# Kernel optimization log

Measured on AMD Instinct MI355X. Metric: run time of the kernel, lower is better.

Reference implementation:

```python
import jax, jax.numpy as jnp
import numpy as np

MARGIN = 0.5
EPS = 1e-12  # matches torch F.normalize eps


def setup_inputs() -> dict:
    key = jax.random.key(0)
    embeddings = jax.random.normal(key, (8192, 256), dtype=jnp.float32)
    return {"embeddings": embeddings}


def reference(embeddings):
    n = embeddings.shape[0]
    # L2-normalize rows (torch F.normalize: x / max(||x||, eps))
    norm = jnp.linalg.norm(embeddings, axis=1, keepdims=True)
    e = embeddings / jnp.maximum(norm, EPS)
    sim = e @ e.T  # [n, n]
    # strict upper triangle mask (i < j)
    iu = jnp.triu(jnp.ones((n, n), dtype=bool), k=1)
    loss_sum = jnp.sum(jnp.where(iu, jax.nn.relu(sim - MARGIN), 0.0))
    count = n * (n - 1) // 2
    return loss_sum / count
```

## Files before the change

### kernel.cpp

```cpp
#include <hip/hip_runtime.h>
#include <hip/hip_fp16.h>

typedef __attribute__((ext_vector_type(4))) float f32x4;
typedef __attribute__((ext_vector_type(8))) int i32x8;

#define NROWS 8192
#define DCOLS 256
#define MARGIN 0.5f
#define NBAND 128
#define NCT 64
#define NBLOCKS 1088

__global__ __launch_bounds__(256) void norm_kernel(const float* __restrict__ x,
                                                   unsigned char* __restrict__ e) {
    const int t = threadIdx.x;
    const int l = t & 63;
    const int c = l & 31;
    const int row = blockIdx.x * 8 + (t >> 6) * 2 + (l >> 5);

    const float4 v0 = *reinterpret_cast<const float4*>(&x[row * DCOLS + c * 8]);
    const float4 v1 = *reinterpret_cast<const float4*>(&x[row * DCOLS + c * 8 + 4]);
    float ss = v0.x * v0.x + v0.y * v0.y + v0.z * v0.z + v0.w * v0.w
             + v1.x * v1.x + v1.y * v1.y + v1.z * v1.z + v1.w * v1.w;
#pragma unroll
    for (int off = 16; off >= 1; off >>= 1) ss += __shfl_xor(ss, off, 32);
    const float inv = 1.0f / fmaxf(sqrtf(ss), 1e-12f);

    const float f[8] = {v0.x, v0.y, v0.z, v0.w, v1.x, v1.y, v1.z, v1.w};
    unsigned int lo = 0, hi = 0;
#pragma unroll
    for (int i = 0; i < 4; ++i) {
        const unsigned short hb = __half_as_ushort(__float2half(f[i] * inv));
        lo |= (unsigned int)(hb >> 8) << (8 * i);
    }
#pragma unroll
    for (int i = 0; i < 4; ++i) {
        const unsigned short hb = __half_as_ushort(__float2half(f[4 + i] * inv));
        hi |= (unsigned int)(hb >> 8) << (8 * i);
    }
    uint2 o; o.x = lo; o.y = hi;
    *reinterpret_cast<uint2*>(e + (size_t)row * DCOLS + c * 8) = o;
}

__global__ __launch_bounds__(256, 4) void tile_kernel(const unsigned char* __restrict__ e,
                                                      float* __restrict__ part) {
    const int orig = blockIdx.x;
    int bb = (orig & 7) * 136 + (orig >> 3);
    int bi = 0, r;
    while (bb >= (r = ((NCT - (bi >> 1)) + 3) >> 2)) { bb -= r; ++bi; }
    const int j0 = (bi >> 1) + bb * 4;
    const int nj = min(4, NCT - j0);
    const int NS = nj * 2;

    __shared__ char lds[40960];
    char* As = lds;
    char* Bw = lds + 8192;

    const int t = threadIdx.x;
    const int l = t & 63;
    const int w = t >> 6;
    const int wn = w;
    const int lr = l & 15;
    const int hk = l >> 4;
    const unsigned char* eA = e + (size_t)bi * 64 * DCOLS;
    char* myB = Bw + w * 8192;

    auto stageB = [&](int s, int slot) {
        const int jt = j0 + (s >> 1);
        const int kb = s & 1;
        const unsigned char* src = e + (size_t)(jt * 128 + wn * 32) * DCOLS + kb * 128;
#pragma unroll
        for (int i = 0; i < 4; ++i) {
            const int u = i * 64 + l;
            const int hk2 = u >> 6, brow = (u >> 1) & 31, half = u & 1;
            __builtin_amdgcn_global_load_lds(
                (const __attribute__((address_space(1))) void*)(src + brow * DCOLS + hk2 * 32 + half * 16),
                (__attribute__((address_space(3))) void*)(myB + slot * 4096 + u * 16), 16, 0, 0);
        }
    };
    auto stageA = [&](int kb) {
#pragma unroll
        for (int i = 0; i < 2; ++i) {
            const int u = i * 256 + t;
            const int hk2 = u >> 7, arow = (u >> 1) & 63, half = u & 1;
            __builtin_amdgcn_global_load_lds(
                (const __attribute__((address_space(1))) void*)(eA + arow * DCOLS + kb * 128 + hk2 * 32 + half * 16),
                (__attribute__((address_space(3))) void*)(As + u * 16), 16, 0, 0);
        }
    };

    stageA(0);
    stageB(0, 0);
    stageB(1, 1);
    asm volatile("s_waitcnt vmcnt(8)" ::: "memory");
    __builtin_amdgcn_s_barrier();
    __builtin_amdgcn_sched_barrier(0);

    i32x8 af[2][4];
#pragma unroll
    for (int m = 0; m < 4; ++m)
        af[0][m] = *reinterpret_cast<const i32x8*>(As + hk * 2048 + (m * 16 + lr) * 32);
    __builtin_amdgcn_s_barrier();
    __builtin_amdgcn_sched_barrier(0);
    stageA(1);
    asm volatile("s_waitcnt vmcnt(0)" ::: "memory");
    __builtin_amdgcn_s_barrier();
    __builtin_amdgcn_sched_barrier(0);
#pragma unroll
    for (int m = 0; m < 4; ++m)
        af[1][m] = *reinterpret_cast<const i32x8*>(As + hk * 2048 + (m * 16 + lr) * 32);

    f32x4 acc[4][2];
#pragma unroll
    for (int m = 0; m < 4; ++m)
#pragma unroll
        for (int n = 0; n < 2; ++n)
            acc[m][n] = (f32x4){0.f, 0.f, 0.f, 0.f};

    float local = 0.0f;
    for (int jx = 0; jx < nj; ++jx) {
        const int jt = j0 + jx;
#pragma unroll
        for (int kb = 0; kb < 2; ++kb) {
            const int s = jx * 2 + kb;
            asm volatile("s_waitcnt vmcnt(4)" ::: "memory");
            i32x8 bf[2];
#pragma unroll
            for (int n = 0; n < 2; ++n)
                bf[n] = *reinterpret_cast<const i32x8*>(
                    myB + (s & 1) * 4096 + hk * 1024 + (n * 16 + lr) * 32);
            asm volatile("s_waitcnt lgkmcnt(0)" ::: "memory");
            __builtin_amdgcn_sched_barrier(0);
            if (s + 2 < NS) stageB(s + 2, s & 1);
            __builtin_amdgcn_s_setprio(1);
#pragma unroll
            for (int m = 0; m < 4; ++m)
#pragma unroll
                for (int n = 0; n < 2; ++n)
                    acc[m][n] = __builtin_amdgcn_mfma_scale_f32_16x16x128_f8f6f4(
                        af[kb][m], bf[n], acc[m][n],
                        1, 1,
                        0, 0x7F7F7F7F,
                        0, 0x7F7F7F7F);
            __builtin_amdgcn_s_setprio(0);
        }
        const int gi0 = bi * 64;
        const int gj0 = jt * 128 + wn * 32;
        if (jt == (bi >> 1)) {
#pragma unroll
            for (int m = 0; m < 4; ++m)
#pragma unroll
                for (int n = 0; n < 2; ++n) {
#pragma unroll
                    for (int r2 = 0; r2 < 4; ++r2) {
                        const int gi = gi0 + m * 16 + hk * 4 + r2;
                        const int gj = gj0 + n * 16 + lr;
                        local += (gi < gj) ? fmaxf(acc[m][n][r2] - MARGIN, 0.0f) : 0.0f;
                    }
                    acc[m][n] = (f32x4){0.f, 0.f, 0.f, 0.f};
                }
        } else {
#pragma unroll
            for (int m = 0; m < 4; ++m)
#pragma unroll
                for (int n = 0; n < 2; ++n) {
#pragma unroll
                    for (int r2 = 0; r2 < 4; ++r2)
                        local += fmaxf(acc[m][n][r2] - MARGIN, 0.0f);
                    acc[m][n] = (f32x4){0.f, 0.f, 0.f, 0.f};
                }
        }
    }

#pragma unroll
    for (int off = 32; off >= 1; off >>= 1) local += __shfl_down(local, off);
    __syncthreads();
    float* red = (float*)lds;
    if (l == 0) red[w] = local;
    __syncthreads();
    if (t == 0) part[orig] = red[0] + red[1] + red[2] + red[3];
}

__global__ __launch_bounds__(256) void fin_kernel(const float* __restrict__ part,
                                                  float* __restrict__ out) {
    __shared__ float red[4];
    const int t = threadIdx.x;
    float v = part[t] + part[t + 256] + part[t + 512] + part[t + 768]
            + (t < NBLOCKS - 1024 ? part[t + 1024] : 0.0f);
#pragma unroll
    for (int off = 32; off >= 1; off >>= 1) v += __shfl_down(v, off);
    if ((t & 63) == 0) red[t >> 6] = v;
    __syncthreads();
    if (t == 0) out[0] = (red[0] + red[1] + red[2] + red[3]) / 33550336.0f;
}

extern "C" void kernel_launch(void* const* d_in, const int* in_sizes, int n_in,
                              void* d_out, int out_size, void* d_ws, size_t ws_size,
                              hipStream_t stream) {
    const float* x = (const float*)d_in[0];
    float* out = (float*)d_out;
    unsigned char* e = (unsigned char*)d_ws;
    float* part = (float*)((char*)d_ws + (size_t)NROWS * DCOLS);

    norm_kernel<<<NROWS / 8, 256, 0, stream>>>(x, e);
    tile_kernel<<<NBLOCKS, 256, 0, stream>>>(e, part);
    fin_kernel<<<1, 256, 0, stream>>>(part, out);
}
```

Baseline: 33.00 us.

## Use 8-wave blocks with shared B tiles and triple-buffered LDS staging

The tile kernel moves from 4 waves that each staged a private 32-row B slice to 8 waves arranged 2x4 that share a common 128-row B tile. The B tile is triple-buffered with barrier-synchronised prefetch, and the whole A tile is loaded once up front. Each wave now holds a 2x2 accumulator block instead of 4x2, which lowers register pressure and raises wave count per block. In exchange it adds a block-wide barrier every k-step, and LDS use grows to about 64KB per block, which may limit how many blocks fit on a CU.

```diff
diff --git a/kernel.cpp b/kernel.cpp
--- a/kernel.cpp
+++ b/kernel.cpp
@@ -2,12 +2,12 @@
 #include <hip/hip_fp16.h>
 
 typedef __attribute__((ext_vector_type(4))) float f32x4;
+typedef __attribute__((ext_vector_type(4))) int i32x4;
 typedef __attribute__((ext_vector_type(8))) int i32x8;
 
 #define NROWS 8192
 #define DCOLS 256
 #define MARGIN 0.5f
-#define NBAND 128
 #define NCT 64
 #define NBLOCKS 1088
 
@@ -42,7 +42,7 @@
     *reinterpret_cast<uint2*>(e + (size_t)row * DCOLS + c * 8) = o;
 }
 
-__global__ __launch_bounds__(256, 4) void tile_kernel(const unsigned char* __restrict__ e,
+__global__ __launch_bounds__(512, 4) void tile_kernel(const unsigned char* __restrict__ e,
                                                       float* __restrict__ part) {
     const int orig = blockIdx.x;
     int bb = (orig & 7) * 136 + (orig >> 3);
@@ -52,103 +52,98 @@
     const int nj = min(4, NCT - j0);
     const int NS = nj * 2;
 
-    __shared__ char lds[40960];
-    char* As = lds;
-    char* Bw = lds + 8192;
+    __shared__ char As[16384];
+    __shared__ char Bs[3][16384];
+    __shared__ float red[8];
 
     const int t = threadIdx.x;
     const int l = t & 63;
     const int w = t >> 6;
-    const int wn = w;
+    const int wm = w >> 2;
+    const int wn = w & 3;
     const int lr = l & 15;
     const int hk = l >> 4;
+
     const unsigned char* eA = e + (size_t)bi * 64 * DCOLS;
-    char* myB = Bw + w * 8192;
 
     auto stageB = [&](int s, int slot) {
-        const int jt = j0 + (s >> 1);
-        const int kb = s & 1;
-        const unsigned char* src = e + (size_t)(jt * 128 + wn * 32) * DCOLS + kb * 128;
-#pragma unroll
-        for (int i = 0; i < 4; ++i) {
-            const int u = i * 64 + l;
-            const int hk2 = u >> 6, brow = (u >> 1) & 31, half = u & 1;
+        const int jt = j0 + (s >> 1), kb = s & 1;
+#pragma unroll
+        for (int i = 0; i < 2; ++i) {
+            const int u = i * 512 + t;
+            const int half = u >> 9, shk = (u >> 7) & 3, brow = u & 127;
             __builtin_amdgcn_global_load_lds(
-                (const __attribute__((address_space(1))) void*)(src + brow * DCOLS + hk2 * 32 + half * 16),
-                (__attribute__((address_space(3))) void*)(myB + slot * 4096 + u * 16), 16, 0, 0);
+                (const __attribute__((address_space(1))) void*)(e
+                    + (size_t)(jt * 128 + brow) * DCOLS + kb * 128 + shk * 32 + half * 16),
+                (__attribute__((address_space(3))) void*)(Bs[slot] + u * 16), 16, 0, 0);
         }
     };
-    auto stageA = [&](int kb) {
-#pragma unroll
-        for (int i = 0; i < 2; ++i) {
-            const int u = i * 256 + t;
-            const int hk2 = u >> 7, arow = (u >> 1) & 63, half = u & 1;
-            __builtin_amdgcn_global_load_lds(
-                (const __attribute__((address_space(1))) void*)(eA + arow * DCOLS + kb * 128 + hk2 * 32 + half * 16),
-                (__attribute__((address_space(3))) void*)(As + u * 16), 16, 0, 0);
-        }
-    };
-
-    stageA(0);
+
+#pragma unroll
+    for (int i = 0; i < 2; ++i) {
+        const int u = i * 512 + t;
+        const int kb = u >> 9, half = (u >> 8) & 1, shk = (u >> 6) & 3, arow = u & 63;
+        __builtin_amdgcn_global_load_lds(
+            (const __attribute__((address_space(1))) void*)(eA + arow * DCOLS + kb * 128 + shk * 32 + half * 16),
+            (__attribute__((address_space(3))) void*)(As + u * 16), 16, 0, 0);
+    }
     stageB(0, 0);
     stageB(1, 1);
-    asm volatile("s_waitcnt vmcnt(8)" ::: "memory");
-    __builtin_amdgcn_s_barrier();
-    __builtin_amdgcn_sched_barrier(0);
-
-    i32x8 af[2][4];
-#pragma unroll
-    for (int m = 0; m < 4; ++m)
-        af[0][m] = *reinterpret_cast<const i32x8*>(As + hk * 2048 + (m * 16 + lr) * 32);
-    __builtin_amdgcn_s_barrier();
-    __builtin_amdgcn_sched_barrier(0);
-    stageA(1);
-    asm volatile("s_waitcnt vmcnt(0)" ::: "memory");
-    __builtin_amdgcn_s_barrier();
-    __builtin_amdgcn_sched_barrier(0);
-#pragma unroll
-    for (int m = 0; m < 4; ++m)
-        af[1][m] = *reinterpret_cast<const i32x8*>(As + hk * 2048 + (m * 16 + lr) * 32);
-
-    f32x4 acc[4][2];
-#pragma unroll
-    for (int m = 0; m < 4; ++m)
+
+    f32x4 acc[2][2];
+#pragma unroll
+    for (int m = 0; m < 2; ++m)
 #pragma unroll
         for (int n = 0; n < 2; ++n)
             acc[m][n] = (f32x4){0.f, 0.f, 0.f, 0.f};
 
+    const int abase = hk * 1024 + (wm * 32 + lr) * 16;
+    const int bbase = hk * 2048 + (wn * 32 + lr) * 16;
+
     float local = 0.0f;
+    int sl = 0;
     for (int jx = 0; jx < nj; ++jx) {
         const int jt = j0 + jx;
 #pragma unroll
         for (int kb = 0; kb < 2; ++kb) {
             const int s = jx * 2 + kb;
-            asm volatile("s_waitcnt vmcnt(4)" ::: "memory");
-            i32x8 bf[2];
-#pragma unroll
-            for (int n = 0; n < 2; ++n)
-                bf[n] = *reinterpret_cast<const i32x8*>(
-                    myB + (s & 1) * 4096 + hk * 1024 + (n * 16 + lr) * 32);
-            asm volatile("s_waitcnt lgkmcnt(0)" ::: "memory");
-            __builtin_amdgcn_sched_barrier(0);
-            if (s + 2 < NS) stageB(s + 2, s & 1);
+            asm volatile("s_waitcnt vmcnt(2)" ::: "memory");
+            __builtin_amdgcn_s_barrier();
+            if (s + 2 < NS) {
+                int sl2 = sl + 2; if (sl2 >= 3) sl2 -= 3;
+                stageB(s + 2, sl2);
+            }
+            i32x8 af[2], bf[2];
+#pragma unroll
+            for (int m = 0; m < 2; ++m) {
+                i32x4 lo = *reinterpret_cast<const i32x4*>(As + kb * 8192 + m * 256 + abase);
+                i32x4 hi = *reinterpret_cast<const i32x4*>(As + kb * 8192 + 4096 + m * 256 + abase);
+                af[m] = (i32x8){lo[0], lo[1], lo[2], lo[3], hi[0], hi[1], hi[2], hi[3]};
+            }
+#pragma unroll
+            for (int n = 0; n < 2; ++n) {
+                i32x4 lo = *reinterpret_cast<const i32x4*>(Bs[sl] + n * 256 + bbase);
+                i32x4 hi = *reinterpret_cast<const i32x4*>(Bs[sl] + 8192 + n * 256 + bbase);
+                bf[n] = (i32x8){lo[0], lo[1], lo[2], lo[3], hi[0], hi[1], hi[2], hi[3]};
+            }
             __builtin_amdgcn_s_setprio(1);
 #pragma unroll
-            for (int m = 0; m < 4; ++m)
+            for (int m = 0; m < 2; ++m)
 #pragma unroll
                 for (int n = 0; n < 2; ++n)
                     acc[m][n] = __builtin_amdgcn_mfma_scale_f32_16x16x128_f8f6f4(
-                        af[kb][m], bf[n], acc[m][n],
+                        af[m], bf[n], acc[m][n],
                         1, 1,
                         0, 0x7F7F7F7F,
                         0, 0x7F7F7F7F);
             __builtin_amdgcn_s_setprio(0);
+            ++sl; if (sl >= 3) sl -= 3;
         }
-        const int gi0 = bi * 64;
+        const int gi0 = bi * 64 + wm * 32;
         const int gj0 = jt * 128 + wn * 32;
         if (jt == (bi >> 1)) {
 #pragma unroll
-            for (int m = 0; m < 4; ++m)
+            for (int m = 0; m < 2; ++m)
 #pragma unroll
                 for (int n = 0; n < 2; ++n) {
 #pragma unroll
@@ -161,7 +156,7 @@
                 }
         } else {
 #pragma unroll
-            for (int m = 0; m < 4; ++m)
+            for (int m = 0; m < 2; ++m)
 #pragma unroll
                 for (int n = 0; n < 2; ++n) {
 #pragma unroll
@@ -174,11 +169,14 @@
 
 #pragma unroll
     for (int off = 32; off >= 1; off >>= 1) local += __shfl_down(local, off);
-    __syncthreads();
-    float* red = (float*)lds;
     if (l == 0) red[w] = local;
     __syncthreads();
-    if (t == 0) part[orig] = red[0] + red[1] + red[2] + red[3];
+    if (t == 0) {
+        float s = 0.0f;
+#pragma unroll
+        for (int i = 0; i < 8; ++i) s += red[i];
+        part[orig] = s;
+    }
 }
 
 __global__ __launch_bounds__(256) void fin_kernel(const float* __restrict__ part,
@@ -203,6 +201,6 @@
     float* part = (float*)((char*)d_ws + (size_t)NROWS * DCOLS);
 
     norm_kernel<<<NROWS / 8, 256, 0, stream>>>(x, e);
-    tile_kernel<<<NBLOCKS, 256, 0, stream>>>(e, part);
+    tile_kernel<<<NBLOCKS, 512, 0, stream>>>(e, part);
     fin_kernel<<<1, 256, 0, stream>>>(part, out);
 }
```

After: 41.64 us. +26.2%, slower.

## Enlarge row band to 128 rows with 2 column tiles per block and triple-buffered B

Applied to the files above, without the earlier changes.

Each block now covers a 128-row A band instead of 64 and walks 2 column tiles instead of 4. This halves B traffic per output and removes the split A staging and barriers by loading all of A up front. B staging moves to a three-slot buffer with an explicitly unrolled schedule, and the per-wave accumulators double. Occupancy drops to 2 blocks per CU because registers and LDS grow, which could reduce latency hiding.

```diff
diff --git a/kernel.cpp b/kernel.cpp
--- a/kernel.cpp
+++ b/kernel.cpp
@@ -7,9 +7,8 @@
 #define NROWS 8192
 #define DCOLS 256
 #define MARGIN 0.5f
-#define NBAND 128
-#define NCT 64
-#define NBLOCKS 1088
+#define NT 64
+#define NBLOCKS 1056
 
 __global__ __launch_bounds__(256) void norm_kernel(const float* __restrict__ x,
                                                    unsigned char* __restrict__ e) {
@@ -42,19 +41,18 @@
     *reinterpret_cast<uint2*>(e + (size_t)row * DCOLS + c * 8) = o;
 }
 
-__global__ __launch_bounds__(256, 4) void tile_kernel(const unsigned char* __restrict__ e,
+__global__ __launch_bounds__(256, 2) void tile_kernel(const unsigned char* __restrict__ e,
                                                       float* __restrict__ part) {
     const int orig = blockIdx.x;
-    int bb = (orig & 7) * 136 + (orig >> 3);
+    int bb = (orig & 7) * 132 + (orig >> 3);
     int bi = 0, r;
-    while (bb >= (r = ((NCT - (bi >> 1)) + 3) >> 2)) { bb -= r; ++bi; }
-    const int j0 = (bi >> 1) + bb * 4;
-    const int nj = min(4, NCT - j0);
-    const int NS = nj * 2;
-
-    __shared__ char lds[40960];
-    char* As = lds;
-    char* Bw = lds + 8192;
+    while (bb >= (r = ((NT - bi) + 1) >> 1)) { bb -= r; ++bi; }
+    const int j0 = bi + bb * 2;
+    const int nj = min(2, NT - j0);
+
+    __shared__ char As[32768];
+    __shared__ char Bw[4][3][4096];
+    __shared__ float red[4];
 
     const int t = threadIdx.x;
     const int l = t & 63;
@@ -62,12 +60,11 @@
     const int wn = w;
     const int lr = l & 15;
     const int hk = l >> 4;
-    const unsigned char* eA = e + (size_t)bi * 64 * DCOLS;
-    char* myB = Bw + w * 8192;
+    const unsigned char* eA = e + (size_t)bi * 128 * DCOLS;
+    char* myB = Bw[w][0];
 
     auto stageB = [&](int s, int slot) {
-        const int jt = j0 + (s >> 1);
-        const int kb = s & 1;
+        const int jt = j0 + (s >> 1), kb = s & 1;
         const unsigned char* src = e + (size_t)(jt * 128 + wn * 32) * DCOLS + kb * 128;
 #pragma unroll
         for (int i = 0; i < 4; ++i) {
@@ -78,77 +75,65 @@
                 (__attribute__((address_space(3))) void*)(myB + slot * 4096 + u * 16), 16, 0, 0);
         }
     };
-    auto stageA = [&](int kb) {
-#pragma unroll
-        for (int i = 0; i < 2; ++i) {
-            const int u = i * 256 + t;
-            const int hk2 = u >> 7, arow = (u >> 1) & 63, half = u & 1;
-            __builtin_amdgcn_global_load_lds(
-                (const __attribute__((address_space(1))) void*)(eA + arow * DCOLS + kb * 128 + hk2 * 32 + half * 16),
-                (__attribute__((address_space(3))) void*)(As + u * 16), 16, 0, 0);
-        }
-    };
-
-    stageA(0);
+
+#pragma unroll
+    for (int i = 0; i < 8; ++i) {
+        const int u = i * 256 + t;
+        const int kb = u >> 10, hk2 = (u >> 8) & 3, arow = (u >> 1) & 127, half = u & 1;
+        __builtin_amdgcn_global_load_lds(
+            (const __attribute__((address_space(1))) void*)(eA + arow * DCOLS + kb * 128 + hk2 * 32 + half * 16),
+            (__attribute__((address_space(3))) void*)(As + u * 16), 16, 0, 0);
+    }
     stageB(0, 0);
     stageB(1, 1);
     asm volatile("s_waitcnt vmcnt(8)" ::: "memory");
     __builtin_amdgcn_s_barrier();
     __builtin_amdgcn_sched_barrier(0);
 
-    i32x8 af[2][4];
-#pragma unroll
-    for (int m = 0; m < 4; ++m)
-        af[0][m] = *reinterpret_cast<const i32x8*>(As + hk * 2048 + (m * 16 + lr) * 32);
-    __builtin_amdgcn_s_barrier();
-    __builtin_amdgcn_sched_barrier(0);
-    stageA(1);
-    asm volatile("s_waitcnt vmcnt(0)" ::: "memory");
-    __builtin_amdgcn_s_barrier();
-    __builtin_amdgcn_sched_barrier(0);
-#pragma unroll
-    for (int m = 0; m < 4; ++m)
-        af[1][m] = *reinterpret_cast<const i32x8*>(As + hk * 2048 + (m * 16 + lr) * 32);
-
-    f32x4 acc[4][2];
-#pragma unroll
-    for (int m = 0; m < 4; ++m)
+    i32x8 af[2][8];
+#pragma unroll
+    for (int kb = 0; kb < 2; ++kb)
+#pragma unroll
+        for (int m = 0; m < 8; ++m)
+            af[kb][m] = *reinterpret_cast<const i32x8*>(
+                As + kb * 16384 + hk * 4096 + (m * 16 + lr) * 32);
+
+    f32x4 acc[8][2];
+#pragma unroll
+    for (int m = 0; m < 8; ++m)
 #pragma unroll
         for (int n = 0; n < 2; ++n)
             acc[m][n] = (f32x4){0.f, 0.f, 0.f, 0.f};
 
     float local = 0.0f;
-    for (int jx = 0; jx < nj; ++jx) {
-        const int jt = j0 + jx;
-#pragma unroll
-        for (int kb = 0; kb < 2; ++kb) {
-            const int s = jx * 2 + kb;
-            asm volatile("s_waitcnt vmcnt(4)" ::: "memory");
-            i32x8 bf[2];
+
+    auto step = [&](int kb, int slot, int gate, int stage_s, int stage_slot) {
+        if (gate == 4) asm volatile("s_waitcnt vmcnt(4)" ::: "memory");
+        else           asm volatile("s_waitcnt vmcnt(0)" ::: "memory");
+        if (stage_s >= 0) stageB(stage_s, stage_slot);
+        i32x8 bf[2];
+#pragma unroll
+        for (int n = 0; n < 2; ++n)
+            bf[n] = *reinterpret_cast<const i32x8*>(
+                myB + slot * 4096 + hk * 1024 + (n * 16 + lr) * 32);
+        __builtin_amdgcn_s_setprio(1);
+#pragma unroll
+        for (int m = 0; m < 8; ++m)
 #pragma unroll
             for (int n = 0; n < 2; ++n)
-                bf[n] = *reinterpret_cast<const i32x8*>(
-                    myB + (s & 1) * 4096 + hk * 1024 + (n * 16 + lr) * 32);
-            asm volatile("s_waitcnt lgkmcnt(0)" ::: "memory");
-            __builtin_amdgcn_sched_barrier(0);
-            if (s + 2 < NS) stageB(s + 2, s & 1);
-            __builtin_amdgcn_s_setprio(1);
-#pragma unroll
-            for (int m = 0; m < 4; ++m)
-#pragma unroll
-                for (int n = 0; n < 2; ++n)
-                    acc[m][n] = __builtin_amdgcn_mfma_scale_f32_16x16x128_f8f6f4(
-                        af[kb][m], bf[n], acc[m][n],
-                        1, 1,
-                        0, 0x7F7F7F7F,
-                        0, 0x7F7F7F7F);
-            __builtin_amdgcn_s_setprio(0);
-        }
-        const int gi0 = bi * 64;
+                acc[m][n] = __builtin_amdgcn_mfma_scale_f32_16x16x128_f8f6f4(
+                    af[kb][m], bf[n], acc[m][n],
+                    1, 1,
+                    0, 0x7F7F7F7F,
+                    0, 0x7F7F7F7F);
+        __builtin_amdgcn_s_setprio(0);
+    };
+    auto finish_tile = [&](int jt) {
+        const int gi0 = bi * 128;
         const int gj0 = jt * 128 + wn * 32;
-        if (jt == (bi >> 1)) {
-#pragma unroll
-            for (int m = 0; m < 4; ++m)
+        if (jt == bi) {
+#pragma unroll
+            for (int m = 0; m < 8; ++m)
 #pragma unroll
                 for (int n = 0; n < 2; ++n) {
 #pragma unroll
@@ -161,7 +146,7 @@
                 }
         } else {
 #pragma unroll
-            for (int m = 0; m < 4; ++m)
+            for (int m = 0; m < 8; ++m)
 #pragma unroll
                 for (int n = 0; n < 2; ++n) {
 #pragma unroll
@@ -170,12 +155,23 @@
                     acc[m][n] = (f32x4){0.f, 0.f, 0.f, 0.f};
                 }
         }
+    };
+
+    if (nj == 2) {
+        step(0, 0, 4, 2, 2);
+        step(1, 1, 4, 3, 0);
+        finish_tile(j0);
+        step(0, 2, 4, -1, 0);
+        step(1, 0, 0, -1, 0);
+        finish_tile(j0 + 1);
+    } else {
+        step(0, 0, 4, -1, 0);
+        step(1, 1, 0, -1, 0);
+        finish_tile(j0);
     }
 
 #pragma unroll
     for (int off = 32; off >= 1; off >>= 1) local += __shfl_down(local, off);
-    __syncthreads();
-    float* red = (float*)lds;
     if (l == 0) red[w] = local;
     __syncthreads();
     if (t == 0) part[orig] = red[0] + red[1] + red[2] + red[3];
```

Result: slower. 38.31 us (+16.1%).
